# Performance work log

Hardware: AMD Instinct MI355X
Metric: run time of the kernel (lower is better)

The kernel has to match this reference:

```python
import jax, jax.numpy as jnp
import numpy as np

D_MODEL = 1024
N_OCTAVES = 3


def _index_maps(d_model: int, n_octaves: int):
    """Static octave index maps, matching HarmonicMixing._build_index_maps."""
    maps = []
    for octave in range(1, n_octaves + 1):
        stride = 2 ** octave
        up_src = np.arange(d_model // stride)
        up_tgt = up_src * stride                      # i -> i*stride
        down_src = np.arange(stride, d_model)
        down_tgt = down_src // stride                 # i -> i // stride (many-to-one)
        maps.append((up_src, up_tgt, down_src, down_tgt))
    return maps


def setup_inputs() -> dict:
    key = jax.random.key(0)
    k1, k2, k3 = jax.random.split(key, 3)
    x = jax.random.normal(k1, (8, 4096, D_MODEL), dtype=jnp.float32)
    up_weights = jax.random.uniform(k2, (N_OCTAVES,), dtype=jnp.float32)
    down_weights = jax.random.uniform(k3, (N_OCTAVES,), dtype=jnp.float32)
    return {"x": x, "up_weights": up_weights, "down_weights": down_weights}


def reference(x, up_weights, down_weights):
    d_model = x.shape[-1]
    maps = _index_maps(d_model, N_OCTAVES)
    out = x
    for o, (up_src, up_tgt, down_src, down_tgt) in enumerate(maps):
        up_w = jax.nn.sigmoid(up_weights[o])
        down_w = jax.nn.sigmoid(down_weights[o])
        # gather -> scale -> scatter-add (duplicate targets accumulate)
        out = out.at[..., up_tgt].add(up_w * x[..., up_src])
        out = out.at[..., down_tgt].add(down_w * x[..., down_src])
    return out
```

## Files before the change

kernel.cpp:

```cpp
#include <hip/hip_runtime.h>


constexpr int D = 1024;

__global__ __launch_bounds__(256) void harmonic_kernel(
    const float* __restrict__ x,
    const float* __restrict__ uwp,
    const float* __restrict__ dwp,
    float* __restrict__ out)
{
    __shared__ float rowlo[512];
    __shared__ float S1[512];
    __shared__ float S2[256];
    __shared__ float S3[128];

    const int t = threadIdx.x;
    const long long base = (long long)blockIdx.x * D;

    const float uw0 = 1.f / (1.f + __expf(-uwp[0]));
    const float uw1 = 1.f / (1.f + __expf(-uwp[1]));
    const float uw2 = 1.f / (1.f + __expf(-uwp[2]));
    const float dw0 = 1.f / (1.f + __expf(-dwp[0]));
    const float dw1 = 1.f / (1.f + __expf(-dwp[1]));
    const float dw2 = 1.f / (1.f + __expf(-dwp[2]));

    const int j0 = t * 4;
    const float4 v = *reinterpret_cast<const float4*>(x + base + j0);

    const float s1a = v.x + v.y;
    const float s1b = v.z + v.w;
    const float s2  = s1a + s1b;
    const float s3  = s2 + __shfl_xor(s2, 1);

    if (t < 128) *reinterpret_cast<float4*>(&rowlo[j0]) = v;
    *reinterpret_cast<float2*>(&S1[2 * t]) = make_float2(s1a, s1b);
    S2[t] = s2;
    if ((t & 1) == 0) S3[t >> 1] = s3;
    __syncthreads();

    float4 r = v;

    const float2 u01 = *reinterpret_cast<const float2*>(&rowlo[2 * t]);
    r.x += uw0 * u01.x;
    r.z += uw0 * u01.y;
    r.x += uw1 * rowlo[t];
    if ((t & 1) == 0) r.x += uw2 * rowlo[t >> 1];

    if (t < 128) {
        const float4 a = *reinterpret_cast<const float4*>(&S1[j0]);
        if (t > 0) r.x += dw0 * a.x;
        r.y += dw0 * a.y;
        r.z += dw0 * a.z;
        r.w += dw0 * a.w;
        if (t < 64) {
            const float4 b = *reinterpret_cast<const float4*>(&S2[j0]);
            if (t > 0) r.x += dw1 * b.x;
            r.y += dw1 * b.y;
            r.z += dw1 * b.z;
            r.w += dw1 * b.w;
            if (t < 32) {
                const float4 c = *reinterpret_cast<const float4*>(&S3[j0]);
                if (t > 0) r.x += dw2 * c.x;
                r.y += dw2 * c.y;
                r.z += dw2 * c.z;
                r.w += dw2 * c.w;
            }
        }
    }

    *reinterpret_cast<float4*>(out + base + j0) = r;
}

extern "C" void kernel_launch(void* const* d_in, const int* in_sizes, int n_in,
                              void* d_out, int out_size, void* d_ws, size_t ws_size,
                              hipStream_t stream) {
    const float* x   = (const float*)d_in[0];
    const float* uwp = (const float*)d_in[1];
    const float* dwp = (const float*)d_in[2];
    float* out = (float*)d_out;
    const int n_rows = in_sizes[0] / D;
    harmonic_kernel<<<n_rows, 256, 0, stream>>>(x, uwp, dwp, out);
}
```

Measured before the change: 220.5 us.

## Process 16 rows per block with double-buffered shared memory and prefetch

Result: slower. 227.2 us (+3.0%).

```diff
diff --git a/kernel.cpp b/kernel.cpp
--- a/kernel.cpp
+++ b/kernel.cpp
@@ -2,6 +2,10 @@
 
 
 constexpr int D = 1024;
+constexpr int ROWS = 16;
+
+typedef float v4f __attribute__((ext_vector_type(4)));
+typedef float v2f __attribute__((ext_vector_type(2)));
 
 __global__ __launch_bounds__(256) void harmonic_kernel(
     const float* __restrict__ x,
@@ -9,13 +13,13 @@
     const float* __restrict__ dwp,
     float* __restrict__ out)
 {
-    __shared__ float rowlo[512];
-    __shared__ float S1[512];
-    __shared__ float S2[256];
-    __shared__ float S3[128];
+    __shared__ float rowlo[2][512];
+    __shared__ float S1[2][512];
+    __shared__ float S2[2][256];
+    __shared__ float S3[2][128];
 
     const int t = threadIdx.x;
-    const long long base = (long long)blockIdx.x * D;
+    const int j0 = t * 4;
 
     const float uw0 = 1.f / (1.f + __expf(-uwp[0]));
     const float uw1 = 1.f / (1.f + __expf(-uwp[1]));
@@ -24,51 +28,68 @@
     const float dw1 = 1.f / (1.f + __expf(-dwp[1]));
     const float dw2 = 1.f / (1.f + __expf(-dwp[2]));
 
-    const int j0 = t * 4;
-    const float4 v = *reinterpret_cast<const float4*>(x + base + j0);
+    const long long row0 = (long long)blockIdx.x * ROWS;
+    const float* xp = x + row0 * D + j0;
+    float* op = out + row0 * D + j0;
 
-    const float s1a = v.x + v.y;
-    const float s1b = v.z + v.w;
-    const float s2  = s1a + s1b;
-    const float s3  = s2 + __shfl_xor(s2, 1);
+    v4f v = __builtin_nontemporal_load(reinterpret_cast<const v4f*>(xp));
 
-    if (t < 128) *reinterpret_cast<float4*>(&rowlo[j0]) = v;
-    *reinterpret_cast<float2*>(&S1[2 * t]) = make_float2(s1a, s1b);
-    S2[t] = s2;
-    if ((t & 1) == 0) S3[t >> 1] = s3;
-    __syncthreads();
+    for (int r = 0; r < ROWS; ++r) {
+        const int b = r & 1;
 
-    float4 r = v;
+        const float s1a = v.x + v.y;
+        const float s1b = v.z + v.w;
+        const float s2  = s1a + s1b;
+        const float s3  = s2 + __shfl_xor(s2, 1);
 
-    const float2 u01 = *reinterpret_cast<const float2*>(&rowlo[2 * t]);
-    r.x += uw0 * u01.x;
-    r.z += uw0 * u01.y;
-    r.x += uw1 * rowlo[t];
-    if ((t & 1) == 0) r.x += uw2 * rowlo[t >> 1];
+        if (t < 128) *reinterpret_cast<v4f*>(&rowlo[b][j0]) = v;
+        v2f s1v; s1v.x = s1a; s1v.y = s1b;
+        *reinterpret_cast<v2f*>(&S1[b][2 * t]) = s1v;
+        S2[b][t] = s2;
+        if ((t & 1) == 0) S3[b][t >> 1] = s3;
 
-    if (t < 128) {
-        const float4 a = *reinterpret_cast<const float4*>(&S1[j0]);
-        if (t > 0) r.x += dw0 * a.x;
-        r.y += dw0 * a.y;
-        r.z += dw0 * a.z;
-        r.w += dw0 * a.w;
-        if (t < 64) {
-            const float4 b = *reinterpret_cast<const float4*>(&S2[j0]);
-            if (t > 0) r.x += dw1 * b.x;
-            r.y += dw1 * b.y;
-            r.z += dw1 * b.z;
-            r.w += dw1 * b.w;
-            if (t < 32) {
-                const float4 c = *reinterpret_cast<const float4*>(&S3[j0]);
-                if (t > 0) r.x += dw2 * c.x;
-                r.y += dw2 * c.y;
-                r.z += dw2 * c.z;
-                r.w += dw2 * c.w;
+        v4f vn;
+        if (r + 1 < ROWS)
+            vn = __builtin_nontemporal_load(
+                reinterpret_cast<const v4f*>(xp + (long long)(r + 1) * D));
+
+        __syncthreads();
+
+        v4f res = v;
+
+        const v2f u01 = *reinterpret_cast<const v2f*>(&rowlo[b][2 * t]);
+        res.x += uw0 * u01.x;
+        res.z += uw0 * u01.y;
+        res.x += uw1 * rowlo[b][t];
+        if ((t & 1) == 0) res.x += uw2 * rowlo[b][t >> 1];
+
+        if (t < 128) {
+            const v4f a = *reinterpret_cast<const v4f*>(&S1[b][j0]);
+            if (t > 0) res.x += dw0 * a.x;
+            res.y += dw0 * a.y;
+            res.z += dw0 * a.z;
+            res.w += dw0 * a.w;
+            if (t < 64) {
+                const v4f c = *reinterpret_cast<const v4f*>(&S2[b][j0]);
+                if (t > 0) res.x += dw1 * c.x;
+                res.y += dw1 * c.y;
+                res.z += dw1 * c.z;
+                res.w += dw1 * c.w;
+                if (t < 32) {
+                    const v4f e = *reinterpret_cast<const v4f*>(&S3[b][j0]);
+                    if (t > 0) res.x += dw2 * e.x;
+                    res.y += dw2 * e.y;
+                    res.z += dw2 * e.z;
+                    res.w += dw2 * e.w;
+                }
             }
         }
+
+        __builtin_nontemporal_store(res,
+            reinterpret_cast<v4f*>(op + (long long)r * D));
+
+        v = vn;
     }
-
-    *reinterpret_cast<float4*>(out + base + j0) = r;
 }
 
 extern "C" void kernel_launch(void* const* d_in, const int* in_sizes, int n_in,
@@ -79,5 +100,6 @@
     const float* dwp = (const float*)d_in[2];
     float* out = (float*)d_out;
     const int n_rows = in_sizes[0] / D;
-    harmonic_kernel<<<n_rows, 256, 0, stream>>>(x, uwp, dwp, out);
+    const int n_blocks = n_rows / ROWS;
+    harmonic_kernel<<<n_blocks, 256, 0, stream>>>(x, uwp, dwp, out);
 }
```
